# Performance work log

Measured on AMD Instinct MI355X. Metric: run time of the kernel, lower is better.

Reference implementation:

```python
import jax, jax.numpy as jnp
import numpy as np

B, D, H, W_, C = 2, 64, 64, 64, 96
EPS = 1e-5


def _merge(t):
    # t: [b, d, h, w, c] -> [b, d/2, h/2, w/2, 8*c], channel blocks ordered
    # by itertools.product(i, j, k): block index = i*4 + j*2 + k.
    b, d, h, w, c = t.shape
    t = t.reshape(b, d // 2, 2, h // 2, 2, w // 2, 2, c)
    t = t.transpose(0, 1, 3, 5, 2, 4, 6, 7)  # i slowest, then j, then k
    return t.reshape(b, d // 2, h // 2, w // 2, 8 * c)


def setup_inputs() -> dict:
    key = jax.random.key(0)
    k1, k2, k3 = jax.random.split(key, 3)
    x = jax.random.normal(k1, (B, D, H, W_, C), dtype=jnp.float32)
    mask = jax.random.bernoulli(k2, 0.7, (B, D, H, W_, 1)).astype(jnp.float32)
    gamma = jnp.ones((8 * C,), dtype=jnp.float32)
    beta = jnp.zeros((8 * C,), dtype=jnp.float32)
    W = (jax.random.normal(k3, (8 * C, 2 * C), dtype=jnp.float32)
         / np.float32(np.sqrt(8 * C)))  # Linear(8*dim, 2*dim, bias=False), stored [in, out]
    return {"x": x, "mask": mask, "gamma": gamma, "beta": beta, "W": W}


def reference(x, mask, gamma, beta, W):
    xm = x * mask  # broadcast of [b,d,h,w,1] mask over channels
    xr = _merge(xm)            # [b, d/2, h/2, w/2, 8c]
    mr = _merge(mask)          # [b, d/2, h/2, w/2, 8]
    mask_out = mr.sum(axis=-1) > 0
    # LayerNorm over last (8c) dim, biased variance, eps=1e-5
    mu = xr.mean(axis=-1, keepdims=True)
    var = jnp.mean(jnp.square(xr - mu), axis=-1, keepdims=True)
    xn = (xr - mu) * jax.lax.rsqrt(var + EPS) * gamma + beta
    out = jnp.einsum('bdhwc,co->bdhwo', xn, W)  # [b, d/2, h/2, w/2, 2*dim]
    return out, mask_out
```

## Files before the change

kernel.cpp:

```cpp
#include <hip/hip_runtime.h>

#define NOUT 192
#define M_TOTAL 65536
#define OUT0 (M_TOTAL * NOUT)
#define CSTRIDE 196

typedef __attribute__((ext_vector_type(8))) short  short8;
typedef __attribute__((ext_vector_type(4))) float  f32x4;
typedef __attribute__((ext_vector_type(4))) unsigned short us4;

__device__ __forceinline__ unsigned short f2bf(float f) {
    union { float f; unsigned u; } a; a.f = f;
    unsigned r = a.u + 0x7FFFu + ((a.u >> 16) & 1u);
    return (unsigned short)(r >> 16);
}

__device__ __forceinline__ void gload16(void* lds, const void* g) {
    __builtin_amdgcn_global_load_lds((const __attribute__((address_space(1))) void*)g,
                                     (__attribute__((address_space(3))) void*)lds, 16, 0, 0);
}

__global__ __launch_bounds__(256) void prepw_kernel(const float* __restrict__ Wm,
                                                    unsigned short* __restrict__ Wb) {
    int t = blockIdx.x * 256 + threadIdx.x;
    if (t >= 24 * 12 * 512) return;
    int e  = t & 7;
    int l  = (t >> 3) & 63;
    int f  = t >> 9;
    int fn = f % 12;
    int ks = f / 12;
    Wb[t] = f2bf(Wm[(ks * 32 + ((l >> 4) << 3) + e) * NOUT + fn * 16 + (l & 15)]);
}

__global__ __launch_bounds__(256, 3) void fused_kernel(
    const float* __restrict__ x, const float* __restrict__ mask,
    const float* __restrict__ gamma, const float* __restrict__ beta,
    const unsigned short* __restrict__ Wb, float* __restrict__ out)
{
    __shared__ __align__(16) float rawf[16 * 768];
    __shared__ __align__(16) float maskLds[16 * 8];

    const int tid = threadIdx.x;
    const int l   = tid & 63;
    const int wv  = tid >> 6;
    const int rowbase = blockIdx.x * 16;

    int bi_[3], ch_[3], vo_[3];
#pragma unroll
    for (int m = 0; m < 3; ++m) {
        const int c8 = (m << 8) + (l << 2);
        const int bi = c8 / 96;
        bi_[m] = bi;
        ch_[m] = c8 - bi * 96;
        vo_[m] = ((bi >> 2) << 12) + (((bi >> 1) & 1) << 6) + (bi & 1);
    }

#pragma unroll
    for (int rr = 0; rr < 4; ++rr) {
        const int r  = (wv << 2) + rr;
        const int rg = rowbase + r;
        const int w2 = rg & 31, h2 = (rg >> 5) & 31, d2 = (rg >> 10) & 31, b = rg >> 15;
        const int vbase = ((b * 64 + d2 * 2) * 64 + h2 * 2) * 64 + w2 * 2;
#pragma unroll
        for (int m = 0; m < 3; ++m)
            gload16(&rawf[r * 768 + (m << 8)],
                    x + (size_t)(vbase + vo_[m]) * 96 + ch_[m]);
    }

    if (tid < 128) {
        const int r = tid >> 3, bi = tid & 7;
        const int rg = rowbase + r;
        const int w2 = rg & 31, h2 = (rg >> 5) & 31, d2 = (rg >> 10) & 31, b = rg >> 15;
        const int vbase = ((b * 64 + d2 * 2) * 64 + h2 * 2) * 64 + w2 * 2;
        maskLds[tid] = mask[vbase + ((bi >> 2) << 12) + (((bi >> 1) & 1) << 6) + (bi & 1)];
    }

    float4 g_[3], be_[3];
#pragma unroll
    for (int m = 0; m < 3; ++m) {
        const int c8 = (m << 8) + (l << 2);
        g_[m]  = *(const float4*)(gamma + c8);
        be_[m] = *(const float4*)(beta  + c8);
    }

    __syncthreads();

    if (tid < 16) {
        float ms = 0.f;
#pragma unroll
        for (int i = 0; i < 8; ++i) ms += maskLds[tid * 8 + i];
        out[OUT0 + rowbase + tid] = (ms > 0.f) ? 1.0f : 0.0f;
    }

    float4 vs[4][3];
    float  s[4], s2[4];
#pragma unroll
    for (int rr = 0; rr < 4; ++rr) {
        const int r = (wv << 2) + rr;
#pragma unroll
        for (int m = 0; m < 3; ++m) {
            float4 v = *(const float4*)&rawf[r * 768 + (m << 8) + (l << 2)];
            const float mk = maskLds[r * 8 + bi_[m]];
            v.x *= mk; v.y *= mk; v.z *= mk; v.w *= mk;
            vs[rr][m] = v;
        }
        float a = 0.f, b2 = 0.f;
#pragma unroll
        for (int m = 0; m < 3; ++m) {
            const float4 v = vs[rr][m];
            a  += (v.x + v.y) + (v.z + v.w);
            b2 += (v.x * v.x + v.y * v.y) + (v.z * v.z + v.w * v.w);
        }
        s[rr] = a; s2[rr] = b2;
    }
#pragma unroll
    for (int off = 32; off >= 1; off >>= 1) {
#pragma unroll
        for (int rr = 0; rr < 4; ++rr) {
            s[rr]  += __shfl_xor(s[rr],  off);
            s2[rr] += __shfl_xor(s2[rr], off);
        }
    }
#pragma unroll
    for (int rr = 0; rr < 4; ++rr) {
        const int r = (wv << 2) + rr;
        const float mu  = s[rr] * (1.f / 768.f);
        const float var = s2[rr] * (1.f / 768.f) - mu * mu;
        const float rs  = rsqrtf(var + 1e-5f);
        char* abase = (char*)rawf + r * 3072;
        const int swz = (r & 7) << 4;
#pragma unroll
        for (int m = 0; m < 3; ++m) {
            const float4 v = vs[rr][m];
            us4 o;
            o.x = f2bf((v.x - mu) * rs * g_[m].x + be_[m].x);
            o.y = f2bf((v.y - mu) * rs * g_[m].y + be_[m].y);
            o.z = f2bf((v.z - mu) * rs * g_[m].z + be_[m].z);
            o.w = f2bf((v.w - mu) * rs * g_[m].w + be_[m].w);
            *(us4*)(abase + (((m << 9) + (l << 3)) ^ swz)) = o;
        }
    }
    __syncthreads();

    f32x4 acc[3] = {};
    const int lrow = l & 15;
    const int kq   = (l >> 4) << 4;
    const int aswz = (lrow & 7) << 4;
    const char* aBase = (const char*)rawf + lrow * 3072;
    const short8* Wv = (const short8*)Wb;
    const int bbase = wv * 192 + l;

#pragma unroll 4
    for (int ks = 0; ks < 24; ++ks) {
        const short8 a  = *(const short8*)(aBase + ((((ks << 6) + kq)) ^ aswz));
        const short8 b0 = Wv[ks * 768 + bbase];
        const short8 b1 = Wv[ks * 768 + bbase + 64];
        const short8 b2 = Wv[ks * 768 + bbase + 128];
        acc[0] = __builtin_amdgcn_mfma_f32_16x16x32_bf16(a, b0, acc[0], 0, 0, 0);
        acc[1] = __builtin_amdgcn_mfma_f32_16x16x32_bf16(a, b1, acc[1], 0, 0, 0);
        acc[2] = __builtin_amdgcn_mfma_f32_16x16x32_bf16(a, b2, acc[2], 0, 0, 0);
    }

    __syncthreads();
    float* Clds = rawf;
#pragma unroll
    for (int c = 0; c < 3; ++c)
#pragma unroll
        for (int j = 0; j < 4; ++j)
            Clds[(((l >> 4) << 2) + j) * CSTRIDE + wv * 48 + c * 16 + lrow] = acc[c][j];
    __syncthreads();

#pragma unroll
    for (int idx = tid; idx < 16 * 48; idx += 256) {
        const int row = idx / 48, c4 = idx % 48;
        *(float4*)&out[(size_t)(rowbase + row) * NOUT + (c4 << 2)] =
            *(const float4*)&Clds[row * CSTRIDE + (c4 << 2)];
    }
}

extern "C" void kernel_launch(void* const* d_in, const int* in_sizes, int n_in,
                              void* d_out, int out_size, void* d_ws, size_t ws_size,
                              hipStream_t stream) {
    const float* x     = (const float*)d_in[0];
    const float* mask  = (const float*)d_in[1];
    const float* gamma = (const float*)d_in[2];
    const float* beta  = (const float*)d_in[3];
    const float* Wm    = (const float*)d_in[4];
    float* out = (float*)d_out;
    unsigned short* Wb = (unsigned short*)d_ws;

    prepw_kernel<<<576, 256, 0, stream>>>(Wm, Wb);
    fused_kernel<<<4096, 256, 0, stream>>>(x, mask, gamma, beta, Wb, out);
}
```

Measured before the change: 92.75 us.

## Process four tiles per block with register double-buffered loads

Each block now handles four 16-row tiles, prefetching the next tile's x and mask values into registers while the current tile is normalised and multiplied. The LDS staging of raw inputs and the output transpose buffer are removed. Only a bf16 A-tile stays in LDS, and the mask reduction uses wave shuffles. The intent is to hide global load latency and cut LDS traffic and footprint. The cost is higher register pressure and less coalesced scalar output stores.

```diff
diff --git a/kernel.cpp b/kernel.cpp
--- a/kernel.cpp
+++ b/kernel.cpp
@@ -3,7 +3,6 @@
 #define NOUT 192
 #define M_TOTAL 65536
 #define OUT0 (M_TOTAL * NOUT)
-#define CSTRIDE 196
 
 typedef __attribute__((ext_vector_type(8))) short  short8;
 typedef __attribute__((ext_vector_type(4))) float  f32x4;
@@ -13,11 +12,6 @@
     union { float f; unsigned u; } a; a.f = f;
     unsigned r = a.u + 0x7FFFu + ((a.u >> 16) & 1u);
     return (unsigned short)(r >> 16);
-}
-
-__device__ __forceinline__ void gload16(void* lds, const void* g) {
-    __builtin_amdgcn_global_load_lds((const __attribute__((address_space(1))) void*)g,
-                                     (__attribute__((address_space(3))) void*)lds, 16, 0, 0);
 }
 
 __global__ __launch_bounds__(256) void prepw_kernel(const float* __restrict__ Wm,
@@ -32,82 +26,62 @@
     Wb[t] = f2bf(Wm[(ks * 32 + ((l >> 4) << 3) + e) * NOUT + fn * 16 + (l & 15)]);
 }
 
-__global__ __launch_bounds__(256, 3) void fused_kernel(
-    const float* __restrict__ x, const float* __restrict__ mask,
-    const float* __restrict__ gamma, const float* __restrict__ beta,
-    const unsigned short* __restrict__ Wb, float* __restrict__ out)
+struct TileData {
+    float4 vs[4][3];
+    float  mval;
+};
+
+__device__ __forceinline__ void load_tile(int tile, const float* __restrict__ x,
+                                          const float* __restrict__ mask,
+                                          int wv, int l,
+                                          const int* ch_, const int* vo_, TileData& td)
 {
-    __shared__ __align__(16) float rawf[16 * 768];
-    __shared__ __align__(16) float maskLds[16 * 8];
-
-    const int tid = threadIdx.x;
-    const int l   = tid & 63;
-    const int wv  = tid >> 6;
-    const int rowbase = blockIdx.x * 16;
-
-    int bi_[3], ch_[3], vo_[3];
-#pragma unroll
-    for (int m = 0; m < 3; ++m) {
-        const int c8 = (m << 8) + (l << 2);
-        const int bi = c8 / 96;
-        bi_[m] = bi;
-        ch_[m] = c8 - bi * 96;
-        vo_[m] = ((bi >> 2) << 12) + (((bi >> 1) & 1) << 6) + (bi & 1);
-    }
-
+    const int rowbase = tile << 4;
 #pragma unroll
     for (int rr = 0; rr < 4; ++rr) {
-        const int r  = (wv << 2) + rr;
-        const int rg = rowbase + r;
+        const int rg = rowbase + (wv << 2) + rr;
         const int w2 = rg & 31, h2 = (rg >> 5) & 31, d2 = (rg >> 10) & 31, b = rg >> 15;
         const int vbase = ((b * 64 + d2 * 2) * 64 + h2 * 2) * 64 + w2 * 2;
 #pragma unroll
         for (int m = 0; m < 3; ++m)
-            gload16(&rawf[r * 768 + (m << 8)],
-                    x + (size_t)(vbase + vo_[m]) * 96 + ch_[m]);
-    }
-
-    if (tid < 128) {
-        const int r = tid >> 3, bi = tid & 7;
-        const int rg = rowbase + r;
+            td.vs[rr][m] = *(const float4*)(x + (size_t)(vbase + vo_[m]) * 96 + ch_[m]);
+    }
+    if (l < 32) {
+        const int rg = rowbase + (wv << 2) + (l >> 3);
         const int w2 = rg & 31, h2 = (rg >> 5) & 31, d2 = (rg >> 10) & 31, b = rg >> 15;
         const int vbase = ((b * 64 + d2 * 2) * 64 + h2 * 2) * 64 + w2 * 2;
-        maskLds[tid] = mask[vbase + ((bi >> 2) << 12) + (((bi >> 1) & 1) << 6) + (bi & 1)];
-    }
-
-    float4 g_[3], be_[3];
-#pragma unroll
-    for (int m = 0; m < 3; ++m) {
-        const int c8 = (m << 8) + (l << 2);
-        g_[m]  = *(const float4*)(gamma + c8);
-        be_[m] = *(const float4*)(beta  + c8);
-    }
-
-    __syncthreads();
-
-    if (tid < 16) {
-        float ms = 0.f;
-#pragma unroll
-        for (int i = 0; i < 8; ++i) ms += maskLds[tid * 8 + i];
-        out[OUT0 + rowbase + tid] = (ms > 0.f) ? 1.0f : 0.0f;
-    }
-
-    float4 vs[4][3];
-    float  s[4], s2[4];
+        const int bi = l & 7;
+        td.mval = mask[vbase + ((bi >> 2) << 12) + (((bi >> 1) & 1) << 6) + (bi & 1)];
+    } else {
+        td.mval = 0.f;
+    }
+}
+
+__device__ __forceinline__ void compute_tile(int tile, TileData& td,
+                                             unsigned short* Alds, const short8* __restrict__ Wv,
+                                             const float4* g_, const float4* be_,
+                                             const int* bi_, int wv, int l,
+                                             float* __restrict__ out)
+{
+    const int rowbase = tile << 4;
+
+    float mo = td.mval;
+    mo = fmaxf(mo, __shfl_xor(mo, 1));
+    mo = fmaxf(mo, __shfl_xor(mo, 2));
+    mo = fmaxf(mo, __shfl_xor(mo, 4));
+    if (l < 32 && (l & 7) == 0)
+        out[OUT0 + rowbase + (wv << 2) + (l >> 3)] = (mo > 0.f) ? 1.f : 0.f;
+
+    float s[4], s2[4];
 #pragma unroll
     for (int rr = 0; rr < 4; ++rr) {
-        const int r = (wv << 2) + rr;
+        float a = 0.f, b2 = 0.f;
 #pragma unroll
         for (int m = 0; m < 3; ++m) {
-            float4 v = *(const float4*)&rawf[r * 768 + (m << 8) + (l << 2)];
-            const float mk = maskLds[r * 8 + bi_[m]];
+            const float mk = __shfl(td.mval, (rr << 3) + bi_[m]);
+            float4 v = td.vs[rr][m];
             v.x *= mk; v.y *= mk; v.z *= mk; v.w *= mk;
-            vs[rr][m] = v;
-        }
-        float a = 0.f, b2 = 0.f;
-#pragma unroll
-        for (int m = 0; m < 3; ++m) {
-            const float4 v = vs[rr][m];
+            td.vs[rr][m] = v;
             a  += (v.x + v.y) + (v.z + v.w);
             b2 += (v.x * v.x + v.y * v.y) + (v.z * v.z + v.w * v.w);
         }
@@ -121,17 +95,18 @@
             s2[rr] += __shfl_xor(s2[rr], off);
         }
     }
+
 #pragma unroll
     for (int rr = 0; rr < 4; ++rr) {
         const int r = (wv << 2) + rr;
         const float mu  = s[rr] * (1.f / 768.f);
         const float var = s2[rr] * (1.f / 768.f) - mu * mu;
         const float rs  = rsqrtf(var + 1e-5f);
-        char* abase = (char*)rawf + r * 3072;
+        char* abase = (char*)Alds + r * 1536;
         const int swz = (r & 7) << 4;
 #pragma unroll
         for (int m = 0; m < 3; ++m) {
-            const float4 v = vs[rr][m];
+            const float4 v = td.vs[rr][m];
             us4 o;
             o.x = f2bf((v.x - mu) * rs * g_[m].x + be_[m].x);
             o.y = f2bf((v.y - mu) * rs * g_[m].y + be_[m].y);
@@ -146,13 +121,11 @@
     const int lrow = l & 15;
     const int kq   = (l >> 4) << 4;
     const int aswz = (lrow & 7) << 4;
-    const char* aBase = (const char*)rawf + lrow * 3072;
-    const short8* Wv = (const short8*)Wb;
+    const char* aBase = (const char*)Alds + lrow * 1536;
     const int bbase = wv * 192 + l;
-
-#pragma unroll 4
+#pragma unroll 6
     for (int ks = 0; ks < 24; ++ks) {
-        const short8 a  = *(const short8*)(aBase + ((((ks << 6) + kq)) ^ aswz));
+        const short8 a  = *(const short8*)(aBase + (((ks << 6) + kq) ^ aswz));
         const short8 b0 = Wv[ks * 768 + bbase];
         const short8 b1 = Wv[ks * 768 + bbase + 64];
         const short8 b2 = Wv[ks * 768 + bbase + 128];
@@ -161,21 +134,55 @@
         acc[2] = __builtin_amdgcn_mfma_f32_16x16x32_bf16(a, b2, acc[2], 0, 0, 0);
     }
 
+    const int colb = wv * 48 + lrow;
+    const int r0   = rowbase + ((l >> 4) << 2);
+#pragma unroll
+    for (int c = 0; c < 3; ++c)
+#pragma unroll
+        for (int j = 0; j < 4; ++j)
+            out[(size_t)(r0 + j) * NOUT + colb + c * 16] = acc[c][j];
     __syncthreads();
-    float* Clds = rawf;
-#pragma unroll
-    for (int c = 0; c < 3; ++c)
-#pragma unroll
-        for (int j = 0; j < 4; ++j)
-            Clds[(((l >> 4) << 2) + j) * CSTRIDE + wv * 48 + c * 16 + lrow] = acc[c][j];
-    __syncthreads();
-
-#pragma unroll
-    for (int idx = tid; idx < 16 * 48; idx += 256) {
-        const int row = idx / 48, c4 = idx % 48;
-        *(float4*)&out[(size_t)(rowbase + row) * NOUT + (c4 << 2)] =
-            *(const float4*)&Clds[row * CSTRIDE + (c4 << 2)];
-    }
+}
+
+__global__ __launch_bounds__(256, 3) void fused_kernel(
+    const float* __restrict__ x, const float* __restrict__ mask,
+    const float* __restrict__ gamma, const float* __restrict__ beta,
+    const unsigned short* __restrict__ Wb, float* __restrict__ out)
+{
+    __shared__ __align__(16) unsigned short Alds[16 * 768];
+
+    const int tid = threadIdx.x;
+    const int l   = tid & 63;
+    const int wv  = tid >> 6;
+
+    int bi_[3], ch_[3], vo_[3];
+#pragma unroll
+    for (int m = 0; m < 3; ++m) {
+        const int c8 = (m << 8) + (l << 2);
+        const int bi = c8 / 96;
+        bi_[m] = bi;
+        ch_[m] = c8 - bi * 96;
+        vo_[m] = ((bi >> 2) << 12) + (((bi >> 1) & 1) << 6) + (bi & 1);
+    }
+    float4 g_[3], be_[3];
+#pragma unroll
+    for (int m = 0; m < 3; ++m) {
+        const int c8 = (m << 8) + (l << 2);
+        g_[m]  = *(const float4*)(gamma + c8);
+        be_[m] = *(const float4*)(beta  + c8);
+    }
+    const short8* Wv = (const short8*)Wb;
+
+    const int t0 = blockIdx.x << 2;
+    TileData tA, tB;
+    load_tile(t0 + 0, x, mask, wv, l, ch_, vo_, tA);
+    load_tile(t0 + 1, x, mask, wv, l, ch_, vo_, tB);
+    compute_tile(t0 + 0, tA, Alds, Wv, g_, be_, bi_, wv, l, out);
+    load_tile(t0 + 2, x, mask, wv, l, ch_, vo_, tA);
+    compute_tile(t0 + 1, tB, Alds, Wv, g_, be_, bi_, wv, l, out);
+    load_tile(t0 + 3, x, mask, wv, l, ch_, vo_, tB);
+    compute_tile(t0 + 2, tA, Alds, Wv, g_, be_, bi_, wv, l, out);
+    compute_tile(t0 + 3, tB, Alds, Wv, g_, be_, bi_, wv, l, out);
 }
 
 extern "C" void kernel_launch(void* const* d_in, const int* in_sizes, int n_in,
@@ -190,5 +197,5 @@
     unsigned short* Wb = (unsigned short*)d_ws;
 
     prepw_kernel<<<576, 256, 0, stream>>>(Wm, Wb);
-    fused_kernel<<<4096, 256, 0, stream>>>(x, mask, gamma, beta, Wb, out);
-}
+    fused_kernel<<<1024, 256, 0, stream>>>(x, mask, gamma, beta, Wb, out);
+}
```

New measurement: 122.7 us. +32.2%, slower.
